# Kernel optimization log

Hardware: AMD Instinct MI355X
Metric: run time of the kernel (lower is better)

Reference implementation:

```python
import jax, jax.numpy as jnp
import numpy as np
from jax import lax

# dims: B batch, L seq len, D channels, N SSM state size
BATCH, L, D, N = 8, 2048, 256, 64
MIN_DELTA = 1e-6
EPS = 1e-6


def setup_inputs() -> dict:
    key = jax.random.key(0)
    k0, k1, k2, k3, k4 = jax.random.split(key, 5)
    x = jax.random.normal(k0, (BATCH, L, D), dtype=jnp.float32)
    # log_A chosen so A = softplus(log_A) is small -> discrete_A^L stays finite in fp32
    log_A = -jax.random.normal(k1, (N, N), dtype=jnp.float32) - 3.0
    Bp = jax.random.normal(k2, (D, N), dtype=jnp.float32) * 0.02
    Cp = jax.random.normal(k3, (D, N), dtype=jnp.float32) * 0.02
    log_delta = jnp.full((D,), -8.0, dtype=jnp.float32)  # dt ~ 3.4e-4 (stability)
    skip_D = jnp.ones((D,), dtype=jnp.float32)
    W_out = jax.random.normal(k4, (D, D), dtype=jnp.float32) * (1.0 / np.sqrt(D))
    b_out = jnp.zeros((D,), dtype=jnp.float32)
    return dict(x=x, log_A=log_A, Bp=Bp, Cp=Cp, log_delta=log_delta,
                skip_D=skip_D, W_out=W_out, b_out=b_out)


def reference(x, log_A, Bp, Cp, log_delta, skip_D, W_out, b_out):
    Bsz, Lx, Dx = x.shape
    # --- discretize ---
    A = jax.nn.softplus(log_A)                                  # [N,N]
    dt = jax.nn.softplus(log_delta) + MIN_DELTA                 # [D]
    dA = jax.vmap(jax.scipy.linalg.expm)(A[None] * dt[:, None, None])  # [D,N,N]
    I = jnp.eye(A.shape[0], dtype=A.dtype)
    X = jnp.linalg.solve(A + EPS * I, Bp.T)                     # [N,D] = A^{-1} B^T
    dB = jnp.einsum('dnm,dm->dn', dA - I, X.T)                  # [D,N]
    # --- kernel k[d,l] = C_d . (dA_d)^l dB_d, via sequential recurrence (same math
    # as the explicit A-power loop, carrying the vector instead of the matrix) ---
    def step(v, _):
        return jnp.einsum('dnm,dm->dn', dA, v), jnp.sum(Cp * v, axis=-1)
    _, ks = lax.scan(step, dB, None, length=Lx)                 # ks: [L,D]
    k = ks.T                                                    # [D,L]
    # --- grouped causal conv1d: y[b,d,t] = sum_tau k[d,tau] x[b,d,t-tau] ---
    w = jnp.flip(k, -1)[:, None, :]                             # [D,1,L]
    y = lax.conv_general_dilated(
        jnp.transpose(x, (0, 2, 1)), w, (1,), [(Lx - 1, 0)],
        dimension_numbers=('NCH', 'OIH', 'NCH'), feature_group_count=Dx)
    y = jnp.transpose(y, (0, 2, 1))                             # [B,L,D]
    return (y + x * skip_D) @ W_out.T + b_out
```

## Files before the change

### kernel.cpp

```cpp
#include <hip/hip_runtime.h>

#define Bz 8
#define Lz 2048
#define Dz 256
#define Nz 64
#define SP 68
#define SA 65
#define SAK 72
#define SKB 136
#define SE 68
#define KE 4
#define KP 7

typedef __attribute__((ext_vector_type(8))) short bf16x8;
typedef __attribute__((ext_vector_type(4))) float f32x4;

__device__ __forceinline__ float softplusf(float x) {
  return (x > 20.f) ? x : log1pf(expf(x));
}

__device__ __forceinline__ unsigned short f2bf(float f) {
  unsigned int u = __float_as_uint(f);
  u += 0x7fffu + ((u >> 16) & 1u);
  return (unsigned short)(u >> 16);
}

__device__ __forceinline__ void pmm_acc(const float* __restrict__ LA,
                                        const float* __restrict__ LB,
                                        float* acc, int n, int q) {
  float arow[64];
#pragma unroll
  for (int mm = 0; mm < 16; ++mm) {
    const float4 a4 = *(const float4*)(LA + n * SP + mm * 4);
    arow[4 * mm + 0] = a4.x; arow[4 * mm + 1] = a4.y;
    arow[4 * mm + 2] = a4.z; arow[4 * mm + 3] = a4.w;
  }
#pragma unroll
  for (int i = 0; i < 16; ++i) acc[i] = 0.f;
#pragma unroll 8
  for (int m = 0; m < 64; ++m) {
    const float4 b0 = *(const float4*)(LB + m * SP + q * 16 + 0);
    const float4 b1 = *(const float4*)(LB + m * SP + q * 16 + 4);
    const float4 b2 = *(const float4*)(LB + m * SP + q * 16 + 8);
    const float4 b3 = *(const float4*)(LB + m * SP + q * 16 + 12);
    const float a = arow[m];
    acc[0]  = fmaf(a, b0.x, acc[0]);  acc[1]  = fmaf(a, b0.y, acc[1]);
    acc[2]  = fmaf(a, b0.z, acc[2]);  acc[3]  = fmaf(a, b0.w, acc[3]);
    acc[4]  = fmaf(a, b1.x, acc[4]);  acc[5]  = fmaf(a, b1.y, acc[5]);
    acc[6]  = fmaf(a, b1.z, acc[6]);  acc[7]  = fmaf(a, b1.w, acc[7]);
    acc[8]  = fmaf(a, b2.x, acc[8]);  acc[9]  = fmaf(a, b2.y, acc[9]);
    acc[10] = fmaf(a, b2.z, acc[10]); acc[11] = fmaf(a, b2.w, acc[11]);
    acc[12] = fmaf(a, b3.x, acc[12]); acc[13] = fmaf(a, b3.y, acc[13]);
    acc[14] = fmaf(a, b3.z, acc[14]); acc[15] = fmaf(a, b3.w, acc[15]);
  }
}

__global__ __launch_bounds__(256) void s4_xt(const float* __restrict__ x,
                                             float* __restrict__ xT,
                                             const float* __restrict__ log_A,
                                             float* __restrict__ Apow) {
  if (blockIdx.x == 0 && blockIdx.y == 0) {
    const int i = blockIdx.z * 512 + threadIdx.x;
    Apow[i] = softplusf(log_A[i]);
    Apow[i + 256] = softplusf(log_A[i + 256]);
  }
  __shared__ float tile[64][69];
  const int t0 = blockIdx.x * 64, d0 = blockIdx.y * 64, b = blockIdx.z;
  const int rr = threadIdx.x >> 4;
  const int c4 = (threadIdx.x & 15) * 4;
#pragma unroll
  for (int p = 0; p < 4; ++p) {
    const int row = p * 16 + rr;
    const float4 v = *(const float4*)(x + ((size_t)b * Lz + t0 + row) * Dz + d0 + c4);
    tile[row][c4 + 0] = v.x; tile[row][c4 + 1] = v.y;
    tile[row][c4 + 2] = v.z; tile[row][c4 + 3] = v.w;
  }
  __syncthreads();
#pragma unroll
  for (int p = 0; p < 4; ++p) {
    const int dd = p * 16 + rr;
    float4 o;
    o.x = tile[c4 + 0][dd]; o.y = tile[c4 + 1][dd];
    o.z = tile[c4 + 2][dd]; o.w = tile[c4 + 3][dd];
    *(float4*)(xT + ((size_t)(d0 + dd) * Bz + b) * Lz + t0 + c4) = o;
  }
}

__global__ __launch_bounds__(256, 1) void s4_buildpow(
    float* __restrict__ Apow, const float* __restrict__ Bp,
    const float* __restrict__ Cp, const float* __restrict__ log_delta,
    float* __restrict__ Gk, float* __restrict__ Qk,
    float* __restrict__ kloc, float* __restrict__ dts) {
  __shared__ float As[Nz * SA];
  __shared__ float Pst[KP + 1][Nz];
  __shared__ float Qst[KE + 1][Nz];
  __shared__ float Pv[Nz], Qv[Nz], dBs[Nz];
  __shared__ float prA[4][Nz + 8], prB[4][Nz + 8];
  __shared__ float zp[KE + 1][17], zs[KE + 1];
  __shared__ alignas(16) float PA[Nz * SP];
  __shared__ alignas(16) float PB[Nz * SP];
  const int tid = threadIdx.x;
  const int d = blockIdx.x;
  const int n = tid & 63, qq = tid >> 6;

  if (d >= Dz) {
    const int role = d - Dz;
#pragma unroll
    for (int i = 0; i < 4; ++i) {
      const int e = (tid + 256 * i) * 4;
      const int r = e >> 6, c = e & 63;
      const float4 v = *(const float4*)(Apow + e);
      *(float4*)&PA[r * SP + c] = v;
      *(float4*)&PB[r * SP + c] = v;
    }
    __syncthreads();
    float acc[16];
    pmm_acc(PA, PB, acc, n, qq);
    if (role == 0) {
      float* O = Apow + (size_t)1 * 4096;
#pragma unroll
      for (int v = 0; v < 4; ++v) {
        float4 o;
        o.x = acc[4 * v]; o.y = acc[4 * v + 1];
        o.z = acc[4 * v + 2]; o.w = acc[4 * v + 3];
        *(float4*)(O + n * 64 + qq * 16 + 4 * v) = o;
      }
      return;
    }
    __syncthreads();
#pragma unroll
    for (int i = 0; i < 16; ++i) {
      PB[n * SP + qq * 16 + i] = acc[i];
      if (role == 2) PA[n * SP + qq * 16 + i] = acc[i];
    }
    __syncthreads();
    pmm_acc(PA, PB, acc, n, qq);
    float* O = Apow + (size_t)(role + 1) * 4096;
#pragma unroll
    for (int v = 0; v < 4; ++v) {
      float4 o;
      o.x = acc[4 * v]; o.y = acc[4 * v + 1];
      o.z = acc[4 * v + 2]; o.w = acc[4 * v + 3];
      *(float4*)(O + n * 64 + qq * 16 + 4 * v) = o;
    }
    return;
  }

  const float dt = softplusf(log_delta[d]) + 1e-6f;
#pragma unroll
  for (int i = 0; i < 4; ++i) {
    const int e = (tid + 256 * i) * 4;
    const int r = e >> 6, c = e & 63;
    const float4 v = *(const float4*)(Apow + e);
    As[r * SA + c] = v.x; As[r * SA + c + 1] = v.y;
    As[r * SA + c + 2] = v.z; As[r * SA + c + 3] = v.w;
  }
  if (tid < 64) {
    const float bv = Bp[d * Nz + tid], cv = Cp[d * Nz + tid];
    Pv[tid] = bv; Pst[0][tid] = bv;
    Qv[tid] = cv; Qst[0][tid] = cv;
  }
  __syncthreads();
#pragma unroll 1
  for (int k = 1; k <= KP; ++k) {
    float pp = 0.f, pq = 0.f;
#pragma unroll
    for (int mm = 0; mm < 16; ++mm) {
      const int m = qq * 16 + mm;
      pp += As[n * SA + m] * Pv[m];
      pq += As[m * SA + n] * Qv[m];
    }
    prA[qq][n] = pp; prB[qq][n] = pq;
    __syncthreads();
    if (tid < 64) {
      const float np = prA[0][tid] + prA[1][tid] + prA[2][tid] + prA[3][tid];
      Pv[tid] = np; Pst[k][tid] = np;
      if (k <= KE) {
        const float nq = prB[0][tid] + prB[1][tid] + prB[2][tid] + prB[3][tid];
        Qv[tid] = nq; Qst[k][tid] = nq;
      }
    }
    __syncthreads();
  }
  const float dtc0 = dt;
  const float dtc1 = dt * dt * 0.5f;
  const float dtc2 = dtc1 * dt * (1.f / 3.f);
  const float dtc3 = dtc2 * dt * 0.25f;
  if (tid < 64) {
    dBs[tid] = dtc0 * Pst[0][tid] + dtc1 * Pst[1][tid] +
               dtc2 * Pst[2][tid] + dtc3 * Pst[3][tid];
#pragma unroll
    for (int k = 0; k <= KE; ++k) {
      Gk[(size_t)d * ((KE + 1) * 64) + k * 64 + tid] =
          dtc0 * Pst[k][tid] + dtc1 * Pst[k + 1][tid] +
          dtc2 * Pst[k + 2][tid] + dtc3 * Pst[k + 3][tid];
      Qk[(size_t)d * ((KE + 1) * 64) + k * 64 + tid] = Qst[k][tid];
    }
  }
  __syncthreads();
  if (tid < (KE + 1) * 16) {
    const int k = tid >> 4, seg = tid & 15;
    float s = 0.f;
#pragma unroll
    for (int i = 0; i < 4; ++i) s += Qst[k][seg * 4 + i] * dBs[seg * 4 + i];
    zp[k][seg] = s;
  }
  __syncthreads();
  if (tid <= KE) {
    float s = 0.f;
#pragma unroll
    for (int seg = 0; seg < 16; ++seg) s += zp[tid][seg];
    zs[tid] = s;
  }
  __syncthreads();
  if (tid < 64) {
    const float rdt = (float)tid * dt;
    float c = 1.f, acc = zs[0];
#pragma unroll
    for (int k = 1; k <= KE; ++k) { c *= rdt / (float)k; acc += c * zs[k]; }
    kloc[d * 64 + tid] = acc;
  }
  if (tid == 0) dts[d] = dt;
}

__global__ __launch_bounds__(512, 1) void s4_scanout(
    const float* __restrict__ xT, const float* __restrict__ Apow,
    const float* __restrict__ Gk, const float* __restrict__ Qk,
    const float* __restrict__ kloc, const float* __restrict__ dts,
    const float* __restrict__ skip_D, unsigned short* __restrict__ yb) {
  __shared__ alignas(16) float SB[32][Bz][64];
  __shared__ alignas(16) char ovl[Nz * SE * 4 * 2];
  __shared__ float Gq[(KE + 1) * Nz];
  __shared__ float CTs[KE + 1][66];
  __shared__ alignas(16) float Sw[Bz][SE];
  __shared__ alignas(16) float Xw[Bz][SE];
  __shared__ alignas(16) unsigned short Msb[64 * SKB];
  __shared__ unsigned short kxb[64];
  float* Es = (float*)ovl;
  float* Us = (float*)(ovl + Nz * SE * 4);
  unsigned short* Zsb = (unsigned short*)ovl;

  const int d = blockIdx.x;
  const int tid = threadIdx.x;
  const int w = tid >> 6;
  const int n = tid & 63;
  const float dt = dts[d];
  if (tid < 65) {
    const float rdt = (float)tid * dt;
    float c = 1.f;
    CTs[0][tid] = 1.f;
#pragma unroll
    for (int k = 1; k <= KE; ++k) { c *= rdt / (float)k; CTs[k][tid] = c; }
  }
  for (int idx = tid; idx < (KE + 1) * 64; idx += 512)
    Gq[idx] = Gk[(size_t)d * ((KE + 1) * 64) + idx];
  {
    float ea[8];
#pragma unroll
    for (int i = 0; i < 8; ++i) ea[i] = 0.f;
    const float dt64 = 64.f * dt;
    float ce = 1.f;
#pragma unroll
    for (int k = 1; k <= KE; ++k) {
      ce *= dt64 / (float)k;
      const float* Ak = Apow + (size_t)(k - 1) * 4096;
#pragma unroll
      for (int i = 0; i < 8; ++i)
        ea[i] = fmaf(ce, Ak[tid + 512 * i], ea[i]);
    }
#pragma unroll
    for (int i = 0; i < 8; ++i) {
      const int e = tid + 512 * i;
      const int r = e >> 6, c = e & 63;
      Es[r * SE + c] = ea[i] + ((r == c) ? 1.f : 0.f);
    }
  }
  __syncthreads();
  {
    const int r = tid >> 3, j0 = (tid & 7) * 8;
    float g0 = Gq[0 * 64 + r], g1 = Gq[1 * 64 + r], g2 = Gq[2 * 64 + r];
    float g3 = Gq[3 * 64 + r], g4 = Gq[4 * 64 + r];
#pragma unroll
    for (int jj = 0; jj < 8; ++jj) {
      const int j = j0 + jj;
      float u = g0 * CTs[0][63 - j];
      u = fmaf(g1, CTs[1][63 - j], u);
      u = fmaf(g2, CTs[2][63 - j], u);
      u = fmaf(g3, CTs[3][63 - j], u);
      u = fmaf(g4, CTs[4][63 - j], u);
      Us[r * SE + j] = u;
    }
  }
  __syncthreads();
  float Erow[64], Urow[64];
#pragma unroll
  for (int mb = 0; mb < 16; ++mb) {
    const float4 e4 = *(const float4*)&Es[n * SE + 4 * mb];
    Erow[4 * mb + 0] = e4.x; Erow[4 * mb + 1] = e4.y;
    Erow[4 * mb + 2] = e4.z; Erow[4 * mb + 3] = e4.w;
    const float4 u4 = *(const float4*)&Us[n * SE + 4 * mb];
    Urow[4 * mb + 0] = u4.x; Urow[4 * mb + 1] = u4.y;
    Urow[4 * mb + 2] = u4.z; Urow[4 * mb + 3] = u4.w;
  }
  const float* xw = xT + ((size_t)d * Bz + w) * (size_t)Lz;
  float s = 0.f;
  float xcur = xw[n];
  float xnxt = xw[64 + n];
#pragma unroll 1
  for (int c = 0; c < 32; ++c) {
    Sw[w][n] = s;
    Xw[w][n] = xcur;
    SB[c][w][n] = s;
    const int cl = (c + 2 < 32) ? (c + 2) : 31;
    const float xnew = xw[cl * 64 + n];
    float a0 = 0.f, a1 = 0.f, a2 = 0.f, a3 = 0.f;
#pragma unroll
    for (int mb = 0; mb < 16; ++mb) {
      const float4 sb = *(const float4*)&Sw[w][4 * mb];
      a0 = fmaf(Erow[4 * mb + 0], sb.x, a0);
      a1 = fmaf(Erow[4 * mb + 1], sb.y, a1);
      a2 = fmaf(Erow[4 * mb + 2], sb.z, a2);
      a3 = fmaf(Erow[4 * mb + 3], sb.w, a3);
    }
#pragma unroll
    for (int jb = 0; jb < 16; ++jb) {
      const float4 xb = *(const float4*)&Xw[w][4 * jb];
      a0 = fmaf(Urow[4 * jb + 0], xb.x, a0);
      a1 = fmaf(Urow[4 * jb + 1], xb.y, a1);
      a2 = fmaf(Urow[4 * jb + 2], xb.z, a2);
      a3 = fmaf(Urow[4 * jb + 3], xb.w, a3);
    }
    s = (a0 + a1) + (a2 + a3);
    xcur = xnxt; xnxt = xnew;
  }
  __syncthreads();

  for (int idx = tid; idx < (KE + 1) * 64; idx += 512)
    Gq[idx] = Qk[(size_t)d * ((KE + 1) * 64) + idx];
  if (tid < 64)
    kxb[tid] = f2bf(kloc[d * 64 + tid] + ((tid == 0) ? skip_D[d] : 0.f));

  const int wave = tid >> 6, lane = tid & 63;
  const int quad = lane >> 4, lq = lane & 15;
  const int g = wave >> 2, wv = wave & 3;
  const float* xd = xT + (size_t)d * Bz * Lz;

#pragma unroll
  for (int i = 0; i < 8; ++i) {
    const int u = tid + 512 * i;
    const int zi = u >> 11, rem = u & 2047;
    const int col = rem >> 5, sub = rem & 31;
    const int k0 = sub * 4;
    const int bb = col & 7, ccl = col >> 3;
    const int cc = zi * 8 + ccl;
    float4 v;
    if (k0 < 64) v = *(const float4*)&SB[cc][bb][k0];
    else v = *(const float4*)(xd + (size_t)bb * Lz + cc * 64 + (k0 - 64));
    ushort4 o;
    o.x = f2bf(v.x); o.y = f2bf(v.y); o.z = f2bf(v.z); o.w = f2bf(v.w);
    *(ushort4*)&Zsb[(size_t)zi * 64 * SKB + col * SKB + k0] = o;
  }
  __syncthreads();

#pragma unroll
  for (int i = 0; i < 8; ++i) {
    const int e = tid + 512 * i;
    const int r = e >> 6, m = e & 63;
    float wv2 = 0.f;
#pragma unroll
    for (int k = 0; k <= KE; ++k) wv2 = fmaf(CTs[k][r + 1], Gq[k * 64 + m], wv2);
    Msb[r * SKB + m] = f2bf(wv2);
  }
#pragma unroll
  for (int i = 0; i < 8; ++i) {
    const int e = tid + 512 * i;
    const int r = e >> 6, j = e & 63;
    Msb[r * SKB + 64 + j] = (j <= r) ? kxb[r - j] : (unsigned short)0;
  }
  __syncthreads();

#pragma unroll 1
  for (int p = 0; p < 2; ++p) {
    f32x4 acc[4];
#pragma unroll
    for (int ni = 0; ni < 4; ++ni)
#pragma unroll
      for (int i = 0; i < 4; ++i) acc[ni][i] = 0.f;
#pragma unroll
    for (int ks = 0; ks < 4; ++ks) {
      const bf16x8 af =
          *(const bf16x8*)&Msb[(wv * 16 + lq) * SKB + ks * 32 + quad * 8];
#pragma unroll
      for (int ni = 0; ni < 4; ++ni) {
        const bf16x8 bfr = *(const bf16x8*)
            &Zsb[(size_t)g * 64 * SKB + (ni * 16 + lq) * SKB + ks * 32 + quad * 8];
        acc[ni] = __builtin_amdgcn_mfma_f32_16x16x32_bf16(af, bfr, acc[ni], 0, 0, 0);
      }
    }
#pragma unroll
    for (int ni = 0; ni < 4; ++ni) {
      const int col = ni * 16 + lq;
      const int bb = col & 7, ccl = col >> 3;
      const int cc = (2 * p + g) * 8 + ccl;
      ushort4 o;
      o.x = f2bf(acc[ni][0]); o.y = f2bf(acc[ni][1]);
      o.z = f2bf(acc[ni][2]); o.w = f2bf(acc[ni][3]);
      *(ushort4*)(yb + ((size_t)d * Bz + bb) * Lz + cc * 64 + wv * 16 + quad * 4) = o;
    }
    if (p == 0) {
      __syncthreads();
#pragma unroll
      for (int i = 0; i < 8; ++i) {
        const int u = tid + 512 * i;
        const int zi = u >> 11, rem = u & 2047;
        const int col = rem >> 5, sub = rem & 31;
        const int k0 = sub * 4;
        const int bb = col & 7, ccl = col >> 3;
        const int cc = (2 + zi) * 8 + ccl;
        float4 v;
        if (k0 < 64) v = *(const float4*)&SB[cc][bb][k0];
        else v = *(const float4*)(xd + (size_t)bb * Lz + cc * 64 + (k0 - 64));
        ushort4 o;
        o.x = f2bf(v.x); o.y = f2bf(v.y); o.z = f2bf(v.z); o.w = f2bf(v.w);
        *(ushort4*)&Zsb[(size_t)zi * 64 * SKB + col * SKB + k0] = o;
      }
      __syncthreads();
    }
  }
}

__global__ __launch_bounds__(256, 2) void s4_gemm5(
    const unsigned short* __restrict__ yb, const float* __restrict__ Wo,
    const float* __restrict__ bo, float* __restrict__ out) {
  __shared__ alignas(16) unsigned short LA[128 * SAK];
  __shared__ alignas(16) unsigned short LB[64 * SAK];
  const int tid = threadIdx.x;
  const int wave = tid >> 6, lane = tid & 63;
  const int quad = lane >> 4, lq = lane & 15;
  const int r0 = blockIdx.x * 128;
  const int c0 = blockIdx.y * 64;
  const int brow = r0 >> 11, t0 = r0 & 2047;
  const int ad = tid & 63;
  const int atg = tid >> 6;
  const int bc = tid >> 2;
  const int bko = tid & 3;
  f32x4 acc[2][4];
#pragma unroll
  for (int mi = 0; mi < 2; ++mi)
#pragma unroll
    for (int ni = 0; ni < 4; ++ni)
#pragma unroll
      for (int i = 0; i < 4; ++i) acc[mi][ni][i] = 0.f;
#pragma unroll 1
  for (int ks = 0; ks < 4; ++ks) {
    const int k0 = ks * 64;
    {
      const unsigned short* src =
          yb + ((size_t)(k0 + ad) * Bz + brow) * Lz + t0 + atg * 32;
#pragma unroll
      for (int h = 0; h < 4; ++h) {
        const bf16x8 v = *(const bf16x8*)(src + h * 8);
#pragma unroll
        for (int j = 0; j < 8; ++j)
          LA[(atg * 32 + h * 8 + j) * SAK + ad] = (unsigned short)v[j];
      }
    }
#pragma unroll
    for (int half = 0; half < 2; ++half) {
      const int kk = half * 32 + bko * 8;
      const float* wsrc = Wo + (size_t)(c0 + bc) * Dz + k0 + kk;
      const float4 w0 = *(const float4*)(wsrc);
      const float4 w1 = *(const float4*)(wsrc + 4);
      bf16x8 wv;
      wv[0] = (short)f2bf(w0.x); wv[1] = (short)f2bf(w0.y);
      wv[2] = (short)f2bf(w0.z); wv[3] = (short)f2bf(w0.w);
      wv[4] = (short)f2bf(w1.x); wv[5] = (short)f2bf(w1.y);
      wv[6] = (short)f2bf(w1.z); wv[7] = (short)f2bf(w1.w);
      *(bf16x8*)&LB[bc * SAK + kk] = wv;
    }
    __syncthreads();
#pragma unroll
    for (int ksub = 0; ksub < 2; ++ksub) {
      bf16x8 af[2], bfr[4];
#pragma unroll
      for (int mi = 0; mi < 2; ++mi)
        af[mi] = *(const bf16x8*)
            &LA[(wave * 32 + mi * 16 + lq) * SAK + ksub * 32 + quad * 8];
#pragma unroll
      for (int ni = 0; ni < 4; ++ni)
        bfr[ni] = *(const bf16x8*)
            &LB[(ni * 16 + lq) * SAK + ksub * 32 + quad * 8];
#pragma unroll
      for (int mi = 0; mi < 2; ++mi)
#pragma unroll
        for (int ni = 0; ni < 4; ++ni)
          acc[mi][ni] = __builtin_amdgcn_mfma_f32_16x16x32_bf16(
              af[mi], bfr[ni], acc[mi][ni], 0, 0, 0);
    }
    __syncthreads();
  }
  float bb[4];
#pragma unroll
  for (int ni = 0; ni < 4; ++ni) bb[ni] = bo[c0 + ni * 16 + lq];
#pragma unroll
  for (int mi = 0; mi < 2; ++mi)
#pragma unroll
    for (int i = 0; i < 4; ++i) {
      const int row = r0 + wave * 32 + mi * 16 + quad * 4 + i;
#pragma unroll
      for (int ni = 0; ni < 4; ++ni)
        out[(size_t)row * Dz + c0 + ni * 16 + lq] = acc[mi][ni][i] + bb[ni];
    }
}

extern "C" void kernel_launch(void* const* d_in, const int* in_sizes, int n_in,
                              void* d_out, int out_size, void* d_ws, size_t ws_size,
                              hipStream_t stream) {
  const float* x         = (const float*)d_in[0];
  const float* log_A     = (const float*)d_in[1];
  const float* Bp        = (const float*)d_in[2];
  const float* Cp        = (const float*)d_in[3];
  const float* log_delta = (const float*)d_in[4];
  const float* skip_D    = (const float*)d_in[5];
  const float* W_out     = (const float*)d_in[6];
  const float* b_out     = (const float*)d_in[7];
  float* out = (float*)d_out;

  float* xT   = (float*)d_ws;
  float* ybf  = xT + (size_t)Dz * Bz * Lz;
  float* S    = ybf + (size_t)Dz * Bz * Lz;
  float* Apow = S + (size_t)Dz * (32 * 8 * 64);
  float* Gk   = Apow + (size_t)8 * 4096;
  float* Qk   = Gk + (size_t)Dz * (KE + 1) * 64;
  float* kloc = Qk + (size_t)Dz * (KE + 1) * 64;
  float* dts  = kloc + (size_t)Dz * 64;
  unsigned short* yb = (unsigned short*)ybf;

  hipLaunchKernelGGL(s4_xt, dim3(Lz / 64, Dz / 64, Bz), dim3(256), 0, stream,
                     x, xT, log_A, Apow);
  hipLaunchKernelGGL(s4_buildpow, dim3(Dz + 3), dim3(256), 0, stream,
                     Apow, Bp, Cp, log_delta, Gk, Qk, kloc, dts);
  hipLaunchKernelGGL(s4_scanout, dim3(Dz), dim3(512), 0, stream,
                     xT, Apow, Gk, Qk, kloc, dts, skip_D, yb);
  hipLaunchKernelGGL(s4_gemm5, dim3((Bz * Lz) / 128, Dz / 64), dim3(256), 0, stream,
                     yb, W_out, b_out, out);
}
```

Baseline: 140.9 us.

## Fuse all four stages into one cooperative kernel with grid syncs

Replaces the transpose, power-building, scan and output GEMM kernels with a single cooperative launch of 256 blocks, separated by grid.sync barriers. Each block now computes A^2 and the matrix exponential terms locally instead of reading precomputed A powers from global memory, and keeps the G/Q/kloc coefficients in shared memory rather than round-tripping them through the workspace. The GEMM stage is retiled so that 256 blocks of 512 threads cover the output. The aim is to remove launch gaps and intermediate global traffic, at the cost of redundant per-block matrix products, only 256 blocks for the transpose and GEMM phases, and grid-wide barrier overhead.

```diff
diff --git a/kernel.cpp b/kernel.cpp
--- a/kernel.cpp
+++ b/kernel.cpp
@@ -1,4 +1,7 @@
 #include <hip/hip_runtime.h>
+#include <hip/hip_cooperative_groups.h>
+
+namespace cg = cooperative_groups;
 
 #define Bz 8
 #define Lz 2048
@@ -12,6 +15,17 @@
 #define KE 4
 #define KP 7
 
+#define O_A    65536
+#define O_A2   82944
+#define O_M3   100352
+#define O_EACC 117760
+#define O_AS   135168
+#define O_CT   151808
+#define O_GS   153152
+#define O_QST  154432
+#define O_KXB  155712
+#define SMEM_BYTES 155840
+
 typedef __attribute__((ext_vector_type(8))) short bf16x8;
 typedef __attribute__((ext_vector_type(4))) float f32x4;
 
@@ -25,159 +39,184 @@
   return (unsigned short)(u >> 16);
 }
 
-__device__ __forceinline__ void pmm_acc(const float* __restrict__ LA,
-                                        const float* __restrict__ LB,
-                                        float* acc, int n, int q) {
-  float arow[64];
-#pragma unroll
-  for (int mm = 0; mm < 16; ++mm) {
-    const float4 a4 = *(const float4*)(LA + n * SP + mm * 4);
-    arow[4 * mm + 0] = a4.x; arow[4 * mm + 1] = a4.y;
-    arow[4 * mm + 2] = a4.z; arow[4 * mm + 3] = a4.w;
-  }
-#pragma unroll
-  for (int i = 0; i < 16; ++i) acc[i] = 0.f;
-#pragma unroll 8
-  for (int m = 0; m < 64; ++m) {
-    const float4 b0 = *(const float4*)(LB + m * SP + q * 16 + 0);
-    const float4 b1 = *(const float4*)(LB + m * SP + q * 16 + 4);
-    const float4 b2 = *(const float4*)(LB + m * SP + q * 16 + 8);
-    const float4 b3 = *(const float4*)(LB + m * SP + q * 16 + 12);
-    const float a = arow[m];
-    acc[0]  = fmaf(a, b0.x, acc[0]);  acc[1]  = fmaf(a, b0.y, acc[1]);
-    acc[2]  = fmaf(a, b0.z, acc[2]);  acc[3]  = fmaf(a, b0.w, acc[3]);
-    acc[4]  = fmaf(a, b1.x, acc[4]);  acc[5]  = fmaf(a, b1.y, acc[5]);
-    acc[6]  = fmaf(a, b1.z, acc[6]);  acc[7]  = fmaf(a, b1.w, acc[7]);
-    acc[8]  = fmaf(a, b2.x, acc[8]);  acc[9]  = fmaf(a, b2.y, acc[9]);
-    acc[10] = fmaf(a, b2.z, acc[10]); acc[11] = fmaf(a, b2.w, acc[11]);
-    acc[12] = fmaf(a, b3.x, acc[12]); acc[13] = fmaf(a, b3.y, acc[13]);
-    acc[14] = fmaf(a, b3.z, acc[14]); acc[15] = fmaf(a, b3.w, acc[15]);
-  }
-}
-
-__global__ __launch_bounds__(256) void s4_xt(const float* __restrict__ x,
-                                             float* __restrict__ xT,
-                                             const float* __restrict__ log_A,
-                                             float* __restrict__ Apow) {
-  if (blockIdx.x == 0 && blockIdx.y == 0) {
-    const int i = blockIdx.z * 512 + threadIdx.x;
-    Apow[i] = softplusf(log_A[i]);
-    Apow[i + 256] = softplusf(log_A[i + 256]);
-  }
-  __shared__ float tile[64][69];
-  const int t0 = blockIdx.x * 64, d0 = blockIdx.y * 64, b = blockIdx.z;
-  const int rr = threadIdx.x >> 4;
-  const int c4 = (threadIdx.x & 15) * 4;
-#pragma unroll
-  for (int p = 0; p < 4; ++p) {
-    const int row = p * 16 + rr;
-    const float4 v = *(const float4*)(x + ((size_t)b * Lz + t0 + row) * Dz + d0 + c4);
-    tile[row][c4 + 0] = v.x; tile[row][c4 + 1] = v.y;
-    tile[row][c4 + 2] = v.z; tile[row][c4 + 3] = v.w;
-  }
-  __syncthreads();
-#pragma unroll
-  for (int p = 0; p < 4; ++p) {
-    const int dd = p * 16 + rr;
-    float4 o;
-    o.x = tile[c4 + 0][dd]; o.y = tile[c4 + 1][dd];
-    o.z = tile[c4 + 2][dd]; o.w = tile[c4 + 3][dd];
-    *(float4*)(xT + ((size_t)(d0 + dd) * Bz + b) * Lz + t0 + c4) = o;
-  }
-}
-
-__global__ __launch_bounds__(256, 1) void s4_buildpow(
-    float* __restrict__ Apow, const float* __restrict__ Bp,
+__global__ __launch_bounds__(512, 2) void s4_mega(
+    const float* __restrict__ x, float* __restrict__ xT,
+    const float* __restrict__ log_A, const float* __restrict__ Bp,
     const float* __restrict__ Cp, const float* __restrict__ log_delta,
-    float* __restrict__ Gk, float* __restrict__ Qk,
-    float* __restrict__ kloc, float* __restrict__ dts) {
-  __shared__ float As[Nz * SA];
-  __shared__ float Pst[KP + 1][Nz];
-  __shared__ float Qst[KE + 1][Nz];
-  __shared__ float Pv[Nz], Qv[Nz], dBs[Nz];
-  __shared__ float prA[4][Nz + 8], prB[4][Nz + 8];
-  __shared__ float zp[KE + 1][17], zs[KE + 1];
-  __shared__ alignas(16) float PA[Nz * SP];
-  __shared__ alignas(16) float PB[Nz * SP];
+    const float* __restrict__ skip_D, const float* __restrict__ Wo,
+    const float* __restrict__ bo, unsigned short* __restrict__ yb,
+    float* __restrict__ out) {
+  __shared__ alignas(16) char smem[SMEM_BYTES];
+  cg::grid_group grid = cg::this_grid();
   const int tid = threadIdx.x;
   const int d = blockIdx.x;
-  const int n = tid & 63, qq = tid >> 6;
-
-  if (d >= Dz) {
-    const int role = d - Dz;
-#pragma unroll
-    for (int i = 0; i < 4; ++i) {
-      const int e = (tid + 256 * i) * 4;
-      const int r = e >> 6, c = e & 63;
-      const float4 v = *(const float4*)(Apow + e);
-      *(float4*)&PA[r * SP + c] = v;
-      *(float4*)&PB[r * SP + c] = v;
-    }
-    __syncthreads();
-    float acc[16];
-    pmm_acc(PA, PB, acc, n, qq);
-    if (role == 0) {
-      float* O = Apow + (size_t)1 * 4096;
-#pragma unroll
-      for (int v = 0; v < 4; ++v) {
+
+  {
+    const int g = tid >> 8, tl = tid & 255;
+    float* tile = (float*)smem + g * (64 * 69);
+    const int rr = tl >> 4, c4 = (tl & 15) * 4;
+#pragma unroll 1
+    for (int it = 0; it < 2; ++it) {
+      const int job = blockIdx.x * 4 + g * 2 + it;
+      const int tt = job & 31, dd = (job >> 5) & 3, b = job >> 7;
+      const int t0 = tt * 64, d0 = dd * 64;
+#pragma unroll
+      for (int p = 0; p < 4; ++p) {
+        const int row = p * 16 + rr;
+        const float4 v =
+            *(const float4*)(x + ((size_t)b * Lz + t0 + row) * Dz + d0 + c4);
+        tile[row * 69 + c4 + 0] = v.x; tile[row * 69 + c4 + 1] = v.y;
+        tile[row * 69 + c4 + 2] = v.z; tile[row * 69 + c4 + 3] = v.w;
+      }
+      __syncthreads();
+#pragma unroll
+      for (int p = 0; p < 4; ++p) {
+        const int dd2 = p * 16 + rr;
         float4 o;
-        o.x = acc[4 * v]; o.y = acc[4 * v + 1];
-        o.z = acc[4 * v + 2]; o.w = acc[4 * v + 3];
-        *(float4*)(O + n * 64 + qq * 16 + 4 * v) = o;
-      }
-      return;
-    }
-    __syncthreads();
-#pragma unroll
-    for (int i = 0; i < 16; ++i) {
-      PB[n * SP + qq * 16 + i] = acc[i];
-      if (role == 2) PA[n * SP + qq * 16 + i] = acc[i];
-    }
-    __syncthreads();
-    pmm_acc(PA, PB, acc, n, qq);
-    float* O = Apow + (size_t)(role + 1) * 4096;
-#pragma unroll
-    for (int v = 0; v < 4; ++v) {
-      float4 o;
-      o.x = acc[4 * v]; o.y = acc[4 * v + 1];
-      o.z = acc[4 * v + 2]; o.w = acc[4 * v + 3];
-      *(float4*)(O + n * 64 + qq * 16 + 4 * v) = o;
-    }
-    return;
-  }
-
+        o.x = tile[(c4 + 0) * 69 + dd2]; o.y = tile[(c4 + 1) * 69 + dd2];
+        o.z = tile[(c4 + 2) * 69 + dd2]; o.w = tile[(c4 + 3) * 69 + dd2];
+        *(float4*)(xT + ((size_t)(d0 + dd2) * Bz + b) * Lz + t0 + c4) = o;
+      }
+      __syncthreads();
+    }
+  }
+  __threadfence();
+  grid.sync();
+
+  float* A_sp = (float*)(smem + O_A);
+  float* A2sp = (float*)(smem + O_A2);
+  float* M3sp = (float*)(smem + O_M3);
+  float* Eacc = (float*)(smem + O_EACC);
+  float* As   = (float*)(smem + O_AS);
+  float (*CTs)[66] = (float(*)[66])(smem + O_CT);
+  float* Gs   = (float*)(smem + O_GS);
+  float* Qst  = (float*)(smem + O_QST);
+  unsigned short* kxb = (unsigned short*)(smem + O_KXB);
+  const int n = tid & 63;
+  const int q8 = tid >> 6;
   const float dt = softplusf(log_delta[d]) + 1e-6f;
-#pragma unroll
-  for (int i = 0; i < 4; ++i) {
-    const int e = (tid + 256 * i) * 4;
+
+  if (tid < 65) {
+    const float rdt = (float)tid * dt;
+    float c = 1.f;
+    CTs[0][tid] = 1.f;
+#pragma unroll
+    for (int k = 1; k <= KE; ++k) { c *= rdt / (float)k; CTs[k][tid] = c; }
+  }
+#pragma unroll
+  for (int j = 0; j < 8; ++j) {
+    const int e = tid * 8 + j;
+    const float av = softplusf(log_A[e]);
     const int r = e >> 6, c = e & 63;
-    const float4 v = *(const float4*)(Apow + e);
-    As[r * SA + c] = v.x; As[r * SA + c + 1] = v.y;
-    As[r * SA + c + 2] = v.z; As[r * SA + c + 3] = v.w;
-  }
+    A_sp[r * SP + c] = av;
+    As[r * SA + c] = av;
+  }
+  __syncthreads();
+
+  {
+    float arow[64];
+#pragma unroll
+    for (int mb = 0; mb < 16; ++mb) {
+      const float4 a4 = *(const float4*)(A_sp + n * SP + 4 * mb);
+      arow[4 * mb + 0] = a4.x; arow[4 * mb + 1] = a4.y;
+      arow[4 * mb + 2] = a4.z; arow[4 * mb + 3] = a4.w;
+    }
+    float a8[8];
+#pragma unroll
+    for (int i = 0; i < 8; ++i) a8[i] = 0.f;
+#pragma unroll 8
+    for (int m = 0; m < 64; ++m) {
+      const float4 b0 = *(const float4*)(A_sp + m * SP + q8 * 8);
+      const float4 b1 = *(const float4*)(A_sp + m * SP + q8 * 8 + 4);
+      const float a = arow[m];
+      a8[0] = fmaf(a, b0.x, a8[0]); a8[1] = fmaf(a, b0.y, a8[1]);
+      a8[2] = fmaf(a, b0.z, a8[2]); a8[3] = fmaf(a, b0.w, a8[3]);
+      a8[4] = fmaf(a, b1.x, a8[4]); a8[5] = fmaf(a, b1.y, a8[5]);
+      a8[6] = fmaf(a, b1.z, a8[6]); a8[7] = fmaf(a, b1.w, a8[7]);
+    }
+    float4 o0, o1;
+    o0.x = a8[0]; o0.y = a8[1]; o0.z = a8[2]; o0.w = a8[3];
+    o1.x = a8[4]; o1.y = a8[5]; o1.z = a8[6]; o1.w = a8[7];
+    *(float4*)(A2sp + n * SP + q8 * 8) = o0;
+    *(float4*)(A2sp + n * SP + q8 * 8 + 4) = o1;
+  }
+  __syncthreads();
+
+  const float dt64 = 64.f * dt;
+  const float ce1 = dt64;
+  const float ce2 = ce1 * dt64 * 0.5f;
+  const float ce3 = ce2 * dt64 * (1.f / 3.f);
+  const float ce4 = ce3 * dt64 * 0.25f;
+#pragma unroll
+  for (int j = 0; j < 8; ++j) {
+    const int e = tid * 8 + j;
+    const int r = e >> 6, c = e & 63;
+    const float a = A_sp[r * SP + c], a2 = A2sp[r * SP + c];
+    Eacc[r * SE + c] = ((r == c) ? 1.f : 0.f) + ce1 * a + ce2 * a2;
+    M3sp[r * SP + c] = ce3 * a + ce4 * a2;
+  }
+  __syncthreads();
+
+  {
+    float arow[64];
+#pragma unroll
+    for (int mb = 0; mb < 16; ++mb) {
+      const float4 a4 = *(const float4*)(M3sp + n * SP + 4 * mb);
+      arow[4 * mb + 0] = a4.x; arow[4 * mb + 1] = a4.y;
+      arow[4 * mb + 2] = a4.z; arow[4 * mb + 3] = a4.w;
+    }
+    float a8[8];
+#pragma unroll
+    for (int i = 0; i < 8; ++i) a8[i] = 0.f;
+#pragma unroll 8
+    for (int m = 0; m < 64; ++m) {
+      const float4 b0 = *(const float4*)(A2sp + m * SP + q8 * 8);
+      const float4 b1 = *(const float4*)(A2sp + m * SP + q8 * 8 + 4);
+      const float a = arow[m];
+      a8[0] = fmaf(a, b0.x, a8[0]); a8[1] = fmaf(a, b0.y, a8[1]);
+      a8[2] = fmaf(a, b0.z, a8[2]); a8[3] = fmaf(a, b0.w, a8[3]);
+      a8[4] = fmaf(a, b1.x, a8[4]); a8[5] = fmaf(a, b1.y, a8[5]);
+      a8[6] = fmaf(a, b1.z, a8[6]); a8[7] = fmaf(a, b1.w, a8[7]);
+    }
+#pragma unroll
+    for (int i = 0; i < 8; ++i) Eacc[n * SE + q8 * 8 + i] += a8[i];
+  }
+  __syncthreads();
+
+  float (*Pst)[Nz] = (float(*)[Nz])(smem + 65536);
+  float* Pv  = (float*)(smem + 67584);
+  float* Qv  = (float*)(smem + 67840);
+  float* dBs = (float*)(smem + 68096);
+  float (*prA)[72] = (float(*)[72])(smem + 68352);
+  float (*prB)[72] = (float(*)[72])(smem + 69504);
+  float (*zp)[17] = (float(*)[17])(smem + 70656);
+  float* zs  = (float*)(smem + 71008);
+
   if (tid < 64) {
     const float bv = Bp[d * Nz + tid], cv = Cp[d * Nz + tid];
     Pv[tid] = bv; Pst[0][tid] = bv;
-    Qv[tid] = cv; Qst[0][tid] = cv;
+    Qv[tid] = cv; Qst[0 * 64 + tid] = cv;
   }
   __syncthreads();
 #pragma unroll 1
   for (int k = 1; k <= KP; ++k) {
-    float pp = 0.f, pq = 0.f;
-#pragma unroll
-    for (int mm = 0; mm < 16; ++mm) {
-      const int m = qq * 16 + mm;
-      pp += As[n * SA + m] * Pv[m];
-      pq += As[m * SA + n] * Qv[m];
-    }
-    prA[qq][n] = pp; prB[qq][n] = pq;
+    if (q8 < 4) {
+      float pp = 0.f, pq = 0.f;
+#pragma unroll
+      for (int mm = 0; mm < 16; ++mm) {
+        const int m = q8 * 16 + mm;
+        pp += As[n * SA + m] * Pv[m];
+        pq += As[m * SA + n] * Qv[m];
+      }
+      prA[q8][n] = pp; prB[q8][n] = pq;
+    }
     __syncthreads();
     if (tid < 64) {
       const float np = prA[0][tid] + prA[1][tid] + prA[2][tid] + prA[3][tid];
       Pv[tid] = np; Pst[k][tid] = np;
       if (k <= KE) {
         const float nq = prB[0][tid] + prB[1][tid] + prB[2][tid] + prB[3][tid];
-        Qv[tid] = nq; Qst[k][tid] = nq;
+        Qv[tid] = nq; Qst[k * 64 + tid] = nq;
       }
     }
     __syncthreads();
@@ -190,19 +229,16 @@
     dBs[tid] = dtc0 * Pst[0][tid] + dtc1 * Pst[1][tid] +
                dtc2 * Pst[2][tid] + dtc3 * Pst[3][tid];
 #pragma unroll
-    for (int k = 0; k <= KE; ++k) {
-      Gk[(size_t)d * ((KE + 1) * 64) + k * 64 + tid] =
-          dtc0 * Pst[k][tid] + dtc1 * Pst[k + 1][tid] +
-          dtc2 * Pst[k + 2][tid] + dtc3 * Pst[k + 3][tid];
-      Qk[(size_t)d * ((KE + 1) * 64) + k * 64 + tid] = Qst[k][tid];
-    }
+    for (int k = 0; k <= KE; ++k)
+      Gs[k * 64 + tid] = dtc0 * Pst[k][tid] + dtc1 * Pst[k + 1][tid] +
+                         dtc2 * Pst[k + 2][tid] + dtc3 * Pst[k + 3][tid];
   }
   __syncthreads();
   if (tid < (KE + 1) * 16) {
     const int k = tid >> 4, seg = tid & 15;
     float s = 0.f;
 #pragma unroll
-    for (int i = 0; i < 4; ++i) s += Qst[k][seg * 4 + i] * dBs[seg * 4 + i];
+    for (int i = 0; i < 4; ++i) s += Qst[k * 64 + seg * 4 + i] * dBs[seg * 4 + i];
     zp[k][seg] = s;
   }
   __syncthreads();
@@ -218,68 +254,14 @@
     float c = 1.f, acc = zs[0];
 #pragma unroll
     for (int k = 1; k <= KE; ++k) { c *= rdt / (float)k; acc += c * zs[k]; }
-    kloc[d * 64 + tid] = acc;
-  }
-  if (tid == 0) dts[d] = dt;
-}
-
-__global__ __launch_bounds__(512, 1) void s4_scanout(
-    const float* __restrict__ xT, const float* __restrict__ Apow,
-    const float* __restrict__ Gk, const float* __restrict__ Qk,
-    const float* __restrict__ kloc, const float* __restrict__ dts,
-    const float* __restrict__ skip_D, unsigned short* __restrict__ yb) {
-  __shared__ alignas(16) float SB[32][Bz][64];
-  __shared__ alignas(16) char ovl[Nz * SE * 4 * 2];
-  __shared__ float Gq[(KE + 1) * Nz];
-  __shared__ float CTs[KE + 1][66];
-  __shared__ alignas(16) float Sw[Bz][SE];
-  __shared__ alignas(16) float Xw[Bz][SE];
-  __shared__ alignas(16) unsigned short Msb[64 * SKB];
-  __shared__ unsigned short kxb[64];
-  float* Es = (float*)ovl;
-  float* Us = (float*)(ovl + Nz * SE * 4);
-  unsigned short* Zsb = (unsigned short*)ovl;
-
-  const int d = blockIdx.x;
-  const int tid = threadIdx.x;
-  const int w = tid >> 6;
-  const int n = tid & 63;
-  const float dt = dts[d];
-  if (tid < 65) {
-    const float rdt = (float)tid * dt;
-    float c = 1.f;
-    CTs[0][tid] = 1.f;
-#pragma unroll
-    for (int k = 1; k <= KE; ++k) { c *= rdt / (float)k; CTs[k][tid] = c; }
-  }
-  for (int idx = tid; idx < (KE + 1) * 64; idx += 512)
-    Gq[idx] = Gk[(size_t)d * ((KE + 1) * 64) + idx];
-  {
-    float ea[8];
-#pragma unroll
-    for (int i = 0; i < 8; ++i) ea[i] = 0.f;
-    const float dt64 = 64.f * dt;
-    float ce = 1.f;
-#pragma unroll
-    for (int k = 1; k <= KE; ++k) {
-      ce *= dt64 / (float)k;
-      const float* Ak = Apow + (size_t)(k - 1) * 4096;
-#pragma unroll
-      for (int i = 0; i < 8; ++i)
-        ea[i] = fmaf(ce, Ak[tid + 512 * i], ea[i]);
-    }
-#pragma unroll
-    for (int i = 0; i < 8; ++i) {
-      const int e = tid + 512 * i;
-      const int r = e >> 6, c = e & 63;
-      Es[r * SE + c] = ea[i] + ((r == c) ? 1.f : 0.f);
-    }
-  }
-  __syncthreads();
+    kxb[tid] = f2bf(acc + ((tid == 0) ? skip_D[d] : 0.f));
+  }
+
+  float* Us = (float*)(smem + O_M3);
   {
     const int r = tid >> 3, j0 = (tid & 7) * 8;
-    float g0 = Gq[0 * 64 + r], g1 = Gq[1 * 64 + r], g2 = Gq[2 * 64 + r];
-    float g3 = Gq[3 * 64 + r], g4 = Gq[4 * 64 + r];
+    const float g0 = Gs[0 * 64 + r], g1 = Gs[1 * 64 + r], g2 = Gs[2 * 64 + r];
+    const float g3 = Gs[3 * 64 + r], g4 = Gs[4 * 64 + r];
 #pragma unroll
     for (int jj = 0; jj < 8; ++jj) {
       const int j = j0 + jj;
@@ -292,59 +274,62 @@
     }
   }
   __syncthreads();
+
+  float* SBp = (float*)smem;
+  float* Sw = (float*)(smem + 73728);
+  float* Xw = (float*)(smem + 75904);
+  const int w = q8;
   float Erow[64], Urow[64];
 #pragma unroll
   for (int mb = 0; mb < 16; ++mb) {
-    const float4 e4 = *(const float4*)&Es[n * SE + 4 * mb];
+    const float4 e4 = *(const float4*)(Eacc + n * SE + 4 * mb);
     Erow[4 * mb + 0] = e4.x; Erow[4 * mb + 1] = e4.y;
     Erow[4 * mb + 2] = e4.z; Erow[4 * mb + 3] = e4.w;
-    const float4 u4 = *(const float4*)&Us[n * SE + 4 * mb];
+    const float4 u4 = *(const float4*)(Us + n * SE + 4 * mb);
     Urow[4 * mb + 0] = u4.x; Urow[4 * mb + 1] = u4.y;
     Urow[4 * mb + 2] = u4.z; Urow[4 * mb + 3] = u4.w;
   }
-  const float* xw = xT + ((size_t)d * Bz + w) * (size_t)Lz;
-  float s = 0.f;
-  float xcur = xw[n];
-  float xnxt = xw[64 + n];
+  {
+    const float* xw = xT + ((size_t)d * Bz + w) * (size_t)Lz;
+    float s = 0.f;
+    float xcur = xw[n];
+    float xnxt = xw[64 + n];
 #pragma unroll 1
-  for (int c = 0; c < 32; ++c) {
-    Sw[w][n] = s;
-    Xw[w][n] = xcur;
-    SB[c][w][n] = s;
-    const int cl = (c + 2 < 32) ? (c + 2) : 31;
-    const float xnew = xw[cl * 64 + n];
-    float a0 = 0.f, a1 = 0.f, a2 = 0.f, a3 = 0.f;
-#pragma unroll
-    for (int mb = 0; mb < 16; ++mb) {
-      const float4 sb = *(const float4*)&Sw[w][4 * mb];
-      a0 = fmaf(Erow[4 * mb + 0], sb.x, a0);
-      a1 = fmaf(Erow[4 * mb + 1], sb.y, a1);
-      a2 = fmaf(Erow[4 * mb + 2], sb.z, a2);
-      a3 = fmaf(Erow[4 * mb + 3], sb.w, a3);
-    }
-#pragma unroll
-    for (int jb = 0; jb < 16; ++jb) {
-      const float4 xb = *(const float4*)&Xw[w][4 * jb];
-      a0 = fmaf(Urow[4 * jb + 0], xb.x, a0);
-      a1 = fmaf(Urow[4 * jb + 1], xb.y, a1);
-      a2 = fmaf(Urow[4 * jb + 2], xb.z, a2);
-      a3 = fmaf(Urow[4 * jb + 3], xb.w, a3);
-    }
-    s = (a0 + a1) + (a2 + a3);
-    xcur = xnxt; xnxt = xnew;
-  }
-  __syncthreads();
-
-  for (int idx = tid; idx < (KE + 1) * 64; idx += 512)
-    Gq[idx] = Qk[(size_t)d * ((KE + 1) * 64) + idx];
-  if (tid < 64)
-    kxb[tid] = f2bf(kloc[d * 64 + tid] + ((tid == 0) ? skip_D[d] : 0.f));
-
-  const int wave = tid >> 6, lane = tid & 63;
+    for (int c = 0; c < 32; ++c) {
+      Sw[w * SE + n] = s;
+      Xw[w * SE + n] = xcur;
+      SBp[(c * 8 + w) * 64 + n] = s;
+      const int cl = (c + 2 < 32) ? (c + 2) : 31;
+      const float xnew = xw[cl * 64 + n];
+      float a0 = 0.f, a1 = 0.f, a2 = 0.f, a3 = 0.f;
+#pragma unroll
+      for (int mb = 0; mb < 16; ++mb) {
+        const float4 sb = *(const float4*)(Sw + w * SE + 4 * mb);
+        a0 = fmaf(Erow[4 * mb + 0], sb.x, a0);
+        a1 = fmaf(Erow[4 * mb + 1], sb.y, a1);
+        a2 = fmaf(Erow[4 * mb + 2], sb.z, a2);
+        a3 = fmaf(Erow[4 * mb + 3], sb.w, a3);
+      }
+#pragma unroll
+      for (int jb = 0; jb < 16; ++jb) {
+        const float4 xb = *(const float4*)(Xw + w * SE + 4 * jb);
+        a0 = fmaf(Urow[4 * jb + 0], xb.x, a0);
+        a1 = fmaf(Urow[4 * jb + 1], xb.y, a1);
+        a2 = fmaf(Urow[4 * jb + 2], xb.z, a2);
+        a3 = fmaf(Urow[4 * jb + 3], xb.w, a3);
+      }
+      s = (a0 + a1) + (a2 + a3);
+      xcur = xnxt; xnxt = xnew;
+    }
+  }
+  __syncthreads();
+
+  unsigned short* Zsb = (unsigned short*)(smem + 65536);
+  unsigned short* Msb = (unsigned short*)(smem + O_EACC);
+  const int wave = q8, lane = tid & 63;
   const int quad = lane >> 4, lq = lane & 15;
-  const int g = wave >> 2, wv = wave & 3;
+  const int g2 = wave >> 2, wv = wave & 3;
   const float* xd = xT + (size_t)d * Bz * Lz;
-
 #pragma unroll
   for (int i = 0; i < 8; ++i) {
     const int u = tid + 512 * i;
@@ -354,21 +339,19 @@
     const int bb = col & 7, ccl = col >> 3;
     const int cc = zi * 8 + ccl;
     float4 v;
-    if (k0 < 64) v = *(const float4*)&SB[cc][bb][k0];
+    if (k0 < 64) v = *(const float4*)(SBp + (cc * 8 + bb) * 64 + k0);
     else v = *(const float4*)(xd + (size_t)bb * Lz + cc * 64 + (k0 - 64));
     ushort4 o;
     o.x = f2bf(v.x); o.y = f2bf(v.y); o.z = f2bf(v.z); o.w = f2bf(v.w);
     *(ushort4*)&Zsb[(size_t)zi * 64 * SKB + col * SKB + k0] = o;
   }
-  __syncthreads();
-
 #pragma unroll
   for (int i = 0; i < 8; ++i) {
     const int e = tid + 512 * i;
     const int r = e >> 6, m = e & 63;
     float wv2 = 0.f;
 #pragma unroll
-    for (int k = 0; k <= KE; ++k) wv2 = fmaf(CTs[k][r + 1], Gq[k * 64 + m], wv2);
+    for (int k = 0; k <= KE; ++k) wv2 = fmaf(CTs[k][r + 1], Qst[k * 64 + m], wv2);
     Msb[r * SKB + m] = f2bf(wv2);
   }
 #pragma unroll
@@ -393,7 +376,7 @@
 #pragma unroll
       for (int ni = 0; ni < 4; ++ni) {
         const bf16x8 bfr = *(const bf16x8*)
-            &Zsb[(size_t)g * 64 * SKB + (ni * 16 + lq) * SKB + ks * 32 + quad * 8];
+            &Zsb[(size_t)g2 * 64 * SKB + (ni * 16 + lq) * SKB + ks * 32 + quad * 8];
         acc[ni] = __builtin_amdgcn_mfma_f32_16x16x32_bf16(af, bfr, acc[ni], 0, 0, 0);
       }
     }
@@ -401,7 +384,7 @@
     for (int ni = 0; ni < 4; ++ni) {
       const int col = ni * 16 + lq;
       const int bb = col & 7, ccl = col >> 3;
-      const int cc = (2 * p + g) * 8 + ccl;
+      const int cc = (2 * p + g2) * 8 + ccl;
       ushort4 o;
       o.x = f2bf(acc[ni][0]); o.y = f2bf(acc[ni][1]);
       o.z = f2bf(acc[ni][2]); o.w = f2bf(acc[ni][3]);
@@ -418,7 +401,7 @@
         const int bb = col & 7, ccl = col >> 3;
         const int cc = (2 + zi) * 8 + ccl;
         float4 v;
-        if (k0 < 64) v = *(const float4*)&SB[cc][bb][k0];
+        if (k0 < 64) v = *(const float4*)(SBp + (cc * 8 + bb) * 64 + k0);
         else v = *(const float4*)(xd + (size_t)bb * Lz + cc * 64 + (k0 - 64));
         ushort4 o;
         o.x = f2bf(v.x); o.y = f2bf(v.y); o.z = f2bf(v.z); o.w = f2bf(v.w);
@@ -427,90 +410,88 @@
       __syncthreads();
     }
   }
-}
-
-__global__ __launch_bounds__(256, 2) void s4_gemm5(
-    const unsigned short* __restrict__ yb, const float* __restrict__ Wo,
-    const float* __restrict__ bo, float* __restrict__ out) {
-  __shared__ alignas(16) unsigned short LA[128 * SAK];
-  __shared__ alignas(16) unsigned short LB[64 * SAK];
-  const int tid = threadIdx.x;
-  const int wave = tid >> 6, lane = tid & 63;
-  const int quad = lane >> 4, lq = lane & 15;
-  const int r0 = blockIdx.x * 128;
-  const int c0 = blockIdx.y * 64;
-  const int brow = r0 >> 11, t0 = r0 & 2047;
-  const int ad = tid & 63;
-  const int atg = tid >> 6;
-  const int bc = tid >> 2;
-  const int bko = tid & 3;
-  f32x4 acc[2][4];
-#pragma unroll
-  for (int mi = 0; mi < 2; ++mi)
-#pragma unroll
-    for (int ni = 0; ni < 4; ++ni)
-#pragma unroll
-      for (int i = 0; i < 4; ++i) acc[mi][ni][i] = 0.f;
+  __threadfence();
+  grid.sync();
+
+  {
+    unsigned short* LA = (unsigned short*)smem;
+    unsigned short* LB = (unsigned short*)(smem + 18432);
+    const int rt = blockIdx.x & 127, cp = blockIdx.x >> 7;
+    const int r0 = rt * 128, c0b = cp * 128;
+    const int brow = r0 >> 11, t0 = r0 & 2047;
+    const int ad = tid & 63;
+    const int atg = tid >> 6;
+    const int bc2 = tid >> 2;
+    const int bko = tid & 3;
+    f32x4 acc[2][4];
+#pragma unroll
+    for (int mi = 0; mi < 2; ++mi)
+#pragma unroll
+      for (int ni = 0; ni < 4; ++ni)
+#pragma unroll
+        for (int i = 0; i < 4; ++i) acc[mi][ni][i] = 0.f;
 #pragma unroll 1
-  for (int ks = 0; ks < 4; ++ks) {
-    const int k0 = ks * 64;
-    {
-      const unsigned short* src =
-          yb + ((size_t)(k0 + ad) * Bz + brow) * Lz + t0 + atg * 32;
-#pragma unroll
-      for (int h = 0; h < 4; ++h) {
-        const bf16x8 v = *(const bf16x8*)(src + h * 8);
-#pragma unroll
-        for (int j = 0; j < 8; ++j)
-          LA[(atg * 32 + h * 8 + j) * SAK + ad] = (unsigned short)v[j];
-      }
-    }
-#pragma unroll
-    for (int half = 0; half < 2; ++half) {
-      const int kk = half * 32 + bko * 8;
-      const float* wsrc = Wo + (size_t)(c0 + bc) * Dz + k0 + kk;
-      const float4 w0 = *(const float4*)(wsrc);
-      const float4 w1 = *(const float4*)(wsrc + 4);
-      bf16x8 wv;
-      wv[0] = (short)f2bf(w0.x); wv[1] = (short)f2bf(w0.y);
-      wv[2] = (short)f2bf(w0.z); wv[3] = (short)f2bf(w0.w);
-      wv[4] = (short)f2bf(w1.x); wv[5] = (short)f2bf(w1.y);
-      wv[6] = (short)f2bf(w1.z); wv[7] = (short)f2bf(w1.w);
-      *(bf16x8*)&LB[bc * SAK + kk] = wv;
-    }
-    __syncthreads();
-#pragma unroll
-    for (int ksub = 0; ksub < 2; ++ksub) {
-      bf16x8 af[2], bfr[4];
-#pragma unroll
-      for (int mi = 0; mi < 2; ++mi)
-        af[mi] = *(const bf16x8*)
-            &LA[(wave * 32 + mi * 16 + lq) * SAK + ksub * 32 + quad * 8];
-#pragma unroll
-      for (int ni = 0; ni < 4; ++ni)
-        bfr[ni] = *(const bf16x8*)
-            &LB[(ni * 16 + lq) * SAK + ksub * 32 + quad * 8];
-#pragma unroll
-      for (int mi = 0; mi < 2; ++mi)
+    for (int ks = 0; ks < 4; ++ks) {
+      const int k0 = ks * 64;
+      {
+        const unsigned short* src =
+            yb + ((size_t)(k0 + ad) * Bz + brow) * Lz + t0 + atg * 16;
+#pragma unroll
+        for (int h = 0; h < 2; ++h) {
+          const bf16x8 v = *(const bf16x8*)(src + h * 8);
+#pragma unroll
+          for (int j = 0; j < 8; ++j)
+            LA[(atg * 16 + h * 8 + j) * SAK + ad] = (unsigned short)v[j];
+        }
+      }
+#pragma unroll
+      for (int half = 0; half < 2; ++half) {
+        const int kk = half * 32 + bko * 8;
+        const float* wsrc = Wo + (size_t)(c0b + bc2) * Dz + k0 + kk;
+        const float4 w0 = *(const float4*)(wsrc);
+        const float4 w1 = *(const float4*)(wsrc + 4);
+        bf16x8 wv8;
+        wv8[0] = (short)f2bf(w0.x); wv8[1] = (short)f2bf(w0.y);
+        wv8[2] = (short)f2bf(w0.z); wv8[3] = (short)f2bf(w0.w);
+        wv8[4] = (short)f2bf(w1.x); wv8[5] = (short)f2bf(w1.y);
+        wv8[6] = (short)f2bf(w1.z); wv8[7] = (short)f2bf(w1.w);
+        *(bf16x8*)&LB[bc2 * SAK + kk] = wv8;
+      }
+      __syncthreads();
+#pragma unroll
+      for (int ksub = 0; ksub < 2; ++ksub) {
+        bf16x8 af[2], bfr[4];
+#pragma unroll
+        for (int mi = 0; mi < 2; ++mi)
+          af[mi] = *(const bf16x8*)
+              &LA[(wv * 32 + mi * 16 + lq) * SAK + ksub * 32 + quad * 8];
 #pragma unroll
         for (int ni = 0; ni < 4; ++ni)
-          acc[mi][ni] = __builtin_amdgcn_mfma_f32_16x16x32_bf16(
-              af[mi], bfr[ni], acc[mi][ni], 0, 0, 0);
-    }
-    __syncthreads();
-  }
-  float bb[4];
-#pragma unroll
-  for (int ni = 0; ni < 4; ++ni) bb[ni] = bo[c0 + ni * 16 + lq];
-#pragma unroll
-  for (int mi = 0; mi < 2; ++mi)
-#pragma unroll
-    for (int i = 0; i < 4; ++i) {
-      const int row = r0 + wave * 32 + mi * 16 + quad * 4 + i;
-#pragma unroll
-      for (int ni = 0; ni < 4; ++ni)
-        out[(size_t)row * Dz + c0 + ni * 16 + lq] = acc[mi][ni][i] + bb[ni];
-    }
+          bfr[ni] = *(const bf16x8*)
+              &LB[(g2 * 64 + ni * 16 + lq) * SAK + ksub * 32 + quad * 8];
+#pragma unroll
+        for (int mi = 0; mi < 2; ++mi)
+#pragma unroll
+          for (int ni = 0; ni < 4; ++ni)
+            acc[mi][ni] = __builtin_amdgcn_mfma_f32_16x16x32_bf16(
+                af[mi], bfr[ni], acc[mi][ni], 0, 0, 0);
+      }
+      __syncthreads();
+    }
+    float bbv[4];
+#pragma unroll
+    for (int ni = 0; ni < 4; ++ni) bbv[ni] = bo[c0b + g2 * 64 + ni * 16 + lq];
+#pragma unroll
+    for (int mi = 0; mi < 2; ++mi)
+#pragma unroll
+      for (int i = 0; i < 4; ++i) {
+        const int row = r0 + wv * 32 + mi * 16 + quad * 4 + i;
+#pragma unroll
+        for (int ni = 0; ni < 4; ++ni)
+          out[(size_t)row * Dz + c0b + g2 * 64 + ni * 16 + lq] =
+              acc[mi][ni][i] + bbv[ni];
+      }
+  }
 }
 
 extern "C" void kernel_launch(void* const* d_in, const int* in_sizes, int n_in,
@@ -526,22 +507,12 @@
   const float* b_out     = (const float*)d_in[7];
   float* out = (float*)d_out;
 
-  float* xT   = (float*)d_ws;
-  float* ybf  = xT + (size_t)Dz * Bz * Lz;
-  float* S    = ybf + (size_t)Dz * Bz * Lz;
-  float* Apow = S + (size_t)Dz * (32 * 8 * 64);
-  float* Gk   = Apow + (size_t)8 * 4096;
-  float* Qk   = Gk + (size_t)Dz * (KE + 1) * 64;
-  float* kloc = Qk + (size_t)Dz * (KE + 1) * 64;
-  float* dts  = kloc + (size_t)Dz * 64;
-  unsigned short* yb = (unsigned short*)ybf;
-
-  hipLaunchKernelGGL(s4_xt, dim3(Lz / 64, Dz / 64, Bz), dim3(256), 0, stream,
-                     x, xT, log_A, Apow);
-  hipLaunchKernelGGL(s4_buildpow, dim3(Dz + 3), dim3(256), 0, stream,
-                     Apow, Bp, Cp, log_delta, Gk, Qk, kloc, dts);
-  hipLaunchKernelGGL(s4_scanout, dim3(Dz), dim3(512), 0, stream,
-                     xT, Apow, Gk, Qk, kloc, dts, skip_D, yb);
-  hipLaunchKernelGGL(s4_gemm5, dim3((Bz * Lz) / 128, Dz / 64), dim3(256), 0, stream,
-                     yb, W_out, b_out, out);
+  float* xT = (float*)d_ws;
+  unsigned short* yb = (unsigned short*)(xT + (size_t)Dz * Bz * Lz);
+
+  void* args[] = {(void*)&x, (void*)&xT, (void*)&log_A, (void*)&Bp,
+                  (void*)&Cp, (void*)&log_delta, (void*)&skip_D,
+                  (void*)&W_out, (void*)&b_out, (void*)&yb, (void*)&out};
+  hipLaunchCooperativeKernel((const void*)s4_mega, dim3(Dz), dim3(512),
+                             args, 0, stream);
 }
```

New measurement: 337.9 us. 140% more time.
